# Optimization experiments

Measured on AMD Instinct MI355X. Metric: run time of the kernel, lower is better.

Reference implementation:

```python
import jax, jax.numpy as jnp
import numpy as np

DIM = 256
NHEADS = 4
HID = 512
B, H, W = 8, 48, 48
EPS = 1e-5


def _ln(x, g, b):
    mu = x.mean(-1, keepdims=True)
    var = ((x - mu) ** 2).mean(-1, keepdims=True)
    return (x - mu) * jax.lax.rsqrt(var + EPS) * g + b


def _mha(x, key_mask, wi, bi, wo, bo):
    # torch nn.MultiheadAttention (batch_first) with key padding restricted to active tokens
    Bn, N, C = x.shape
    hd = C // NHEADS
    qkv = x @ wi.T + bi  # [B,N,3C]
    q, k, v = jnp.split(qkv, 3, axis=-1)
    sh = lambda t: t.reshape(Bn, N, NHEADS, hd).transpose(0, 2, 1, 3)  # [B,h,N,hd]
    q, k, v = sh(q), sh(k), sh(v)
    scores = jnp.einsum('bhqd,bhkd->bhqk', q, k) / np.float32(np.sqrt(hd))
    scores = jnp.where(key_mask[:, None, None, :], scores, jnp.float32(-1e9))
    attn = jax.nn.softmax(scores, axis=-1)
    out = jnp.einsum('bhqk,bhkd->bhqd', attn, v)
    out = out.transpose(0, 2, 1, 3).reshape(Bn, N, C)
    return out @ wo.T + bo


def _mixer(x, key_mask, ln_g, ln_b, in_w, in_b, out_w, out_b, f1_w, f1_b, f2_w, f2_b):
    # MixerBlock: shared LayerNorm used before attn and before FFN
    xn = _ln(x, ln_g, ln_b)
    x = x + _mha(xn, key_mask, in_w, in_b, out_w, out_b)
    h = _ln(x, ln_g, ln_b)
    h = jax.nn.gelu(h @ f1_w.T + f1_b, approximate=False) @ f2_w.T + f2_b
    return x + h


def _forward(f_ir, f_vis, agent_w1, agent_b1, bn_gamma, bn_beta, bn_mean, bn_var,
             agent_w2, agent_b2, hyp_w1, hyp_b1, hyp_w2, hyp_b2,
             mir_ln_g, mir_ln_b, mir_in_w, mir_in_b, mir_out_w, mir_out_b,
             mir_f1_w, mir_f1_b, mir_f2_w, mir_f2_b,
             mvis_ln_g, mvis_ln_b, mvis_in_w, mvis_in_b, mvis_out_w, mvis_out_b,
             mvis_f1_w, mvis_f1_b, mvis_f2_w, mvis_f2_b, highlight_scale):
    Bn, C, Hh, Ww = f_ir.shape
    N = Hh * Ww
    base = f_ir + f_vis

    # SamplingAgent (1x1 convs as einsum, BatchNorm in eval mode)
    x = jnp.concatenate([f_ir, f_vis], axis=1)  # [B,2C,H,W]
    h = jnp.einsum('oc,bchw->bohw', agent_w1, x) + agent_b1[None, :, None, None]
    h = (h - bn_mean[None, :, None, None]) * jax.lax.rsqrt(bn_var[None, :, None, None] + EPS)
    h = h * bn_gamma[None, :, None, None] + bn_beta[None, :, None, None]
    h = jax.nn.relu(h)
    logits = jnp.einsum('oc,bchw->bohw', agent_w2, h) + agent_b2[None, :, None, None]
    w_driver = jax.nn.sigmoid(logits)  # [B,1,H,W]; eval path: driver = student

    # HyperNetwork threshold
    g = w_driver.mean(axis=(2, 3))  # [B,1]
    t = jax.nn.sigmoid(jax.nn.relu(g @ hyp_w1.T + hyp_b1) @ hyp_w2.T + hyp_b2)  # [B,1]

    wflat = w_driver.reshape(Bn, N)
    soft = jax.nn.sigmoid((wflat - t) * 50.0)  # [B,N]

    # active set: soft_mask > 0.5, fallback to top-64 of weights when too few
    active = soft > 0.5
    count = active.sum(axis=1)
    _, idx64 = jax.lax.top_k(wflat, 64)
    m64 = jnp.zeros((Bn, N), dtype=bool).at[jnp.arange(Bn)[:, None], idx64].set(True)
    active = jnp.where((count >= 64)[:, None], active, m64)

    tok_ir = f_ir.reshape(Bn, C, N).transpose(0, 2, 1)   # [B,N,C]
    tok_vis = f_vis.reshape(Bn, C, N).transpose(0, 2, 1)
    tok_base = base.reshape(Bn, C, N).transpose(0, 2, 1)

    refined_ir = _mixer(tok_ir, active, mir_ln_g, mir_ln_b, mir_in_w, mir_in_b,
                        mir_out_w, mir_out_b, mir_f1_w, mir_f1_b, mir_f2_w, mir_f2_b)
    refined_vis = _mixer(tok_vis, active, mvis_ln_g, mvis_ln_b, mvis_in_w, mvis_in_b,
                         mvis_out_w, mvis_out_b, mvis_f1_w, mvis_f1_b, mvis_f2_w, mvis_f2_b)

    wsel = wflat[..., None]
    fusion = refined_ir * wsel + refined_vis * (1.0 - wsel)
    delta = fusion * soft[..., None]
    mod = 1.0 + soft[..., None] * highlight_scale
    final = jnp.where(active[..., None], (tok_base + delta) * mod, tok_base)  # scatter-back
    f_final = final.transpose(0, 2, 1).reshape(Bn, C, Hh, Ww)
    aux_loss = jnp.float32(0.0)
    return f_final, aux_loss


def setup_inputs() -> dict:
    key = jax.random.key(0)
    ks = jax.random.split(key, 32)
    C = DIM
    S = 0.02
    r = lambda i, shape, s=S: jax.random.normal(ks[i], shape, dtype=jnp.float32) * s

    def mixer_params(prefix, k0):
        return {
            prefix + '_ln_g': jnp.ones((C,), jnp.float32),
            prefix + '_ln_b': jnp.zeros((C,), jnp.float32),
            prefix + '_in_w': r(k0, (3 * C, C)),
            prefix + '_in_b': jnp.zeros((3 * C,), jnp.float32),
            prefix + '_out_w': r(k0 + 1, (C, C)),
            prefix + '_out_b': jnp.zeros((C,), jnp.float32),
            prefix + '_f1_w': r(k0 + 2, (4 * C, C)),
            prefix + '_f1_b': jnp.zeros((4 * C,), jnp.float32),
            prefix + '_f2_w': r(k0 + 3, (C, 4 * C)),
            prefix + '_f2_b': jnp.zeros((C,), jnp.float32),
        }

    inp = {
        'f_ir': jax.random.normal(ks[0], (B, C, H, W), dtype=jnp.float32),
        'f_vis': jax.random.normal(ks[1], (B, C, H, W), dtype=jnp.float32),
        'agent_w1': r(2, (HID, 2 * C)),
        'agent_b1': jnp.zeros((HID,), jnp.float32),
        'bn_gamma': jnp.ones((HID,), jnp.float32),
        'bn_beta': jnp.zeros((HID,), jnp.float32),
        'bn_mean': jnp.zeros((HID,), jnp.float32),
        'bn_var': jnp.ones((HID,), jnp.float32),
        'agent_w2': r(3, (1, HID)),
        'agent_b2': jnp.zeros((1,), jnp.float32),
        'hyp_w1': r(4, (16, 1), 0.5),
        'hyp_b1': jnp.zeros((16,), jnp.float32),
        'hyp_w2': r(5, (1, 16), 0.5),
        'hyp_b2': jnp.zeros((1,), jnp.float32),
        'highlight_scale': jnp.float32(1.0),
    }
    inp.update(mixer_params('mir', 6))
    inp.update(mixer_params('mvis', 10))
    return inp


def reference(f_ir, f_vis, agent_w1, agent_b1, bn_gamma, bn_beta, bn_mean, bn_var,
              agent_w2, agent_b2, hyp_w1, hyp_b1, hyp_w2, hyp_b2,
              mir_ln_g, mir_ln_b, mir_in_w, mir_in_b, mir_out_w, mir_out_b,
              mir_f1_w, mir_f1_b, mir_f2_w, mir_f2_b,
              mvis_ln_g, mvis_ln_b, mvis_in_w, mvis_in_b, mvis_out_w, mvis_out_b,
              mvis_f1_w, mvis_f1_b, mvis_f2_w, mvis_f2_b, highlight_scale):
    return _forward(f_ir, f_vis, agent_w1, agent_b1, bn_gamma, bn_beta, bn_mean, bn_var,
                    agent_w2, agent_b2, hyp_w1, hyp_b1, hyp_w2, hyp_b2,
                    mir_ln_g, mir_ln_b, mir_in_w, mir_in_b, mir_out_w, mir_out_b,
                    mir_f1_w, mir_f1_b, mir_f2_w, mir_f2_b,
                    mvis_ln_g, mvis_ln_b, mvis_in_w, mvis_in_b, mvis_out_w, mvis_out_b,
                    mvis_f1_w, mvis_f1_b, mvis_f2_w, mvis_f2_b, highlight_scale)
```

## Files before the change

kernel.cpp:

```cpp
#include <hip/hip_runtime.h>
#include <hip/hip_bf16.h>
#include <cstdint>
#include <cstddef>

typedef __attribute__((ext_vector_type(8))) short short8;
typedef __attribute__((ext_vector_type(4))) short s16x4;
typedef __attribute__((ext_vector_type(4))) float f32x4;

#define DEVI static __device__ __forceinline__

constexpr int NB   = 8;
constexpr int CDIM = 256;
constexpr int NTOK = 2304;
constexpr int BNT  = NB * NTOK;
constexpr int HIDN = 512;
constexpr int RCAP = 4096;
constexpr size_t BNTC = (size_t)BNT * CDIM;
constexpr size_t KVSTR = (size_t)32 * NTOK * 64;
constexpr size_t HSTR  = (size_t)BNT * 1024;

DEVI unsigned short f2bf(float f) {
  unsigned u = __builtin_bit_cast(unsigned, f);
  unsigned r = 0x7FFFu + ((u >> 16) & 1u);
  return (unsigned short)((u + r) >> 16);
}
DEVI float bf2f(unsigned short h) {
  unsigned u = ((unsigned)h) << 16;
  return __builtin_bit_cast(float, u);
}

__global__ __launch_bounds__(256) void convert_weights(
    const float* __restrict__ miw, const float* __restrict__ mow,
    const float* __restrict__ mf1, const float* __restrict__ mf2,
    const float* __restrict__ viw, const float* __restrict__ vow,
    const float* __restrict__ vf1, const float* __restrict__ vf2,
    unsigned short* __restrict__ dst)
{
  int i = blockIdx.x * 256 + threadIdx.x;
  int m = i / 786432;
  int r = i % 786432;
  const float* src; int off;
  if      (r < 196608) { src = m ? viw : miw; off = r; }
  else if (r < 262144) { src = m ? vow : mow; off = r - 196608; }
  else if (r < 524288) { src = m ? vf1 : mf1; off = r - 262144; }
  else                 { src = m ? vf2 : mf2; off = r - 524288; }
  dst[i] = f2bf(src[off]);
}

__global__ __launch_bounds__(256) void split_w_kernel(
    const float* __restrict__ w1, unsigned short* __restrict__ W2)
{
  int i = blockIdx.x * 256 + threadIdx.x;
  int n = i >> 9, k = i & 511;
  float v = w1[i];
  unsigned short hi = f2bf(v);
  float r1 = v - bf2f(hi);
  unsigned short mid = f2bf(r1);
  size_t base = (size_t)n * 1024 + k;
  W2[base] = hi; W2[base + 512] = mid;
}

__global__ __launch_bounds__(256) void split_x_kernel(
    const float* __restrict__ f_ir, const float* __restrict__ f_vis,
    unsigned short* __restrict__ A2)
{
  __shared__ float tile[64][65];
  int n0 = blockIdx.x * 64, c0 = blockIdx.y * 64, b = blockIdx.z;
  int tid = threadIdx.x;
  const float* src = (c0 < 256) ? f_ir : f_vis;
  int cc0 = c0 & 255;
#pragma unroll
  for (int i = 0; i < 16; ++i) {
    int l = tid + i * 256;
    int r = l >> 6, col = l & 63;
    tile[r][col] = src[((size_t)b * 256 + cc0 + r) * NTOK + n0 + col];
  }
  __syncthreads();
#pragma unroll
  for (int i = 0; i < 16; ++i) {
    int l = tid + i * 256;
    int r = l >> 6, col = l & 63;
    A2[((size_t)b * NTOK + n0 + r) * 512 + c0 + col] = f2bf(tile[col][r]);
  }
}

__global__ __launch_bounds__(256) void agent_gemm(
    const unsigned short* __restrict__ A2, const unsigned short* __restrict__ W2,
    const float* __restrict__ b1,
    const float* __restrict__ bng, const float* __restrict__ bnb,
    const float* __restrict__ bnm, const float* __restrict__ bnv,
    const float* __restrict__ w2, float* __restrict__ hpart)
{
  __shared__ unsigned short As[128][72];
  __shared__ unsigned short Ws[128][72];
  __shared__ float scl[64], shl[64], w2l[64];
  int tid = threadIdx.x;
  int lane = tid & 63, wid = tid >> 6;
  int wm = (wid >> 1) * 64, wn = (wid & 1) * 32;
  int m0 = blockIdx.x * 128, n0 = blockIdx.y * 64;
  if (tid < 64) {
    int n = n0 + tid;
    double inv = 1.0 / sqrt((double)bnv[n] + 1e-5);
    double sc = (double)bng[n] * inv;
    scl[tid] = (float)sc;
    shl[tid] = (float)(((double)b1[n] - (double)bnm[n]) * sc + (double)bnb[n]);
    w2l[tid] = w2[n];
  }
  f32x4 zero = {0.f, 0.f, 0.f, 0.f};
  f32x4 acc[4][2];
#pragma unroll
  for (int i = 0; i < 4; ++i)
#pragma unroll
    for (int j = 0; j < 2; ++j) acc[i][j] = zero;

  for (int kin = 0; kin < 512; kin += 64) {
    __syncthreads();
#pragma unroll
    for (int i = 0; i < 4; ++i) {
      int l = tid + i * 256;
      int r = l >> 3, ch = (l & 7) * 8;
      *(short8*)&As[r][ch] = *(const short8*)&A2[(size_t)(m0 + r) * 512 + kin + ch];
    }
#pragma unroll
    for (int i = 0; i < 4; ++i) {
      int l = tid + i * 256;
      int r = l >> 3, ch = (l & 7) * 8;
      int wr = (r < 64) ? r : (r - 64);
      int wo = (r < 64) ? 0 : 512;
      *(short8*)&Ws[r][ch] = *(const short8*)&W2[(size_t)(n0 + wr) * 1024 + wo + kin + ch];
    }
    __syncthreads();
#pragma unroll
    for (int ks = 0; ks < 2; ++ks) {
      short8 a[4], bh[2], bm[2];
#pragma unroll
      for (int i = 0; i < 4; ++i)
        a[i] = *(const short8*)&As[wm + i * 16 + (lane & 15)][ks * 32 + (lane >> 4) * 8];
#pragma unroll
      for (int j = 0; j < 2; ++j) {
        bh[j] = *(const short8*)&Ws[wn + j * 16 + (lane & 15)][ks * 32 + (lane >> 4) * 8];
        bm[j] = *(const short8*)&Ws[64 + wn + j * 16 + (lane & 15)][ks * 32 + (lane >> 4) * 8];
      }
#pragma unroll
      for (int i = 0; i < 4; ++i)
#pragma unroll
        for (int j = 0; j < 2; ++j) {
          acc[i][j] = __builtin_amdgcn_mfma_f32_16x16x32_bf16(a[i], bh[j], acc[i][j], 0, 0, 0);
          acc[i][j] = __builtin_amdgcn_mfma_f32_16x16x32_bf16(a[i], bm[j], acc[i][j], 0, 0, 0);
        }
    }
  }

  int rbase = (lane >> 4) * 4;
  int cbase = lane & 15;
  float part[4][4];
#pragma unroll
  for (int i = 0; i < 4; ++i) {
#pragma unroll
    for (int r = 0; r < 4; ++r) {
      float p = 0.f;
#pragma unroll
      for (int j = 0; j < 2; ++j) {
        int nl = wn + j * 16 + cbase;
        float val = acc[i][j][r] * scl[nl] + shl[nl];
        if (val > 0.f) p += val * w2l[nl];
      }
      part[i][r] = p;
    }
  }
#pragma unroll
  for (int msk = 1; msk < 16; msk <<= 1) {
#pragma unroll
    for (int i = 0; i < 4; ++i)
#pragma unroll
      for (int r = 0; r < 4; ++r)
        part[i][r] += __shfl_xor(part[i][r], msk);
  }
  if (cbase == 0) {
    int slot = blockIdx.y * 2 + (wid & 1);
#pragma unroll
    for (int i = 0; i < 4; ++i)
#pragma unroll
      for (int r = 0; r < 4; ++r) {
        int mm = m0 + wm + i * 16 + rbase + r;
        hpart[(size_t)mm * 16 + slot] = part[i][r];
      }
  }
}

__global__ __launch_bounds__(256) void decide_kernel(
    const float* __restrict__ hpart, const float* __restrict__ b2,
    const float* __restrict__ hw1, const float* __restrict__ hb1,
    const float* __restrict__ hw2, const float* __restrict__ hb2,
    double* __restrict__ w64, float* __restrict__ w32, double* __restrict__ t64,
    int* __restrict__ rcount, int* __restrict__ rlist)
{
  __shared__ double red[256];
  __shared__ double tsh;
  int b = blockIdx.x, tid = threadIdx.x;
  double wloc[9];
  double s = 0.0;
#pragma unroll
  for (int c = 0; c < 9; ++c) {
    int pix = b * NTOK + c * 256 + tid;
    const float* hp = hpart + (size_t)pix * 16;
    double lg = (double)b2[0];
#pragma unroll
    for (int j = 0; j < 16; ++j) lg += (double)hp[j];
    double wd = 1.0 / (1.0 + exp(-lg));
    w64[pix] = wd; w32[pix] = (float)wd;
    wloc[c] = wd;
    s += wd;
  }
  red[tid] = s;
  __syncthreads();
  for (int st = 128; st; st >>= 1) {
    if (tid < st) red[tid] += red[tid + st];
    __syncthreads();
  }
  if (tid == 0) {
    double g = red[0] / 2304.0;
    double acc = (double)hb2[0];
    for (int j = 0; j < 16; ++j) {
      double hh = g * (double)hw1[j] + (double)hb1[j];
      hh = hh > 0.0 ? hh : 0.0;
      acc += hh * (double)hw2[j];
    }
    tsh = 1.0 / (1.0 + exp(-acc));
    t64[b] = tsh;
  }
  __syncthreads();
  double t = tsh;
#pragma unroll
  for (int c = 0; c < 9; ++c) {
    if (fabs(wloc[c] - t) < 1.5e-3) {
      int pix = b * NTOK + c * 256 + tid;
      int idx = atomicAdd(rcount, 1);
      if (idx < RCAP) rlist[idx] = pix;
    }
  }
}

__global__ __launch_bounds__(256) void refine_kernel(
    const float* __restrict__ f_ir, const float* __restrict__ f_vis,
    const float* __restrict__ w1, const float* __restrict__ b1,
    const float* __restrict__ bng, const float* __restrict__ bnb,
    const float* __restrict__ bnm, const float* __restrict__ bnv,
    const float* __restrict__ w2, const float* __restrict__ b2,
    const int* __restrict__ rlist, const int* __restrict__ rcount,
    double* __restrict__ w64, float* __restrict__ w32)
{
  int nr = rcount[0]; if (nr > RCAP) nr = RCAP;
  if ((int)blockIdx.x >= nr) return;
  int pix = rlist[blockIdx.x];
  int b = pix / NTOK, n = pix % NTOK;
  __shared__ double xs[512];
  __shared__ double scs[512], shs[512];
  __shared__ double lred[4];
  int tid = threadIdx.x, lane = tid & 63, wid = tid >> 6;
  xs[tid]       = (double)f_ir [((size_t)b * 256 + tid) * NTOK + n];
  xs[256 + tid] = (double)f_vis[((size_t)b * 256 + tid) * NTOK + n];
#pragma unroll
  for (int h = 0; h < 2; ++h) {
    int o = tid + h * 256;
    double inv = 1.0 / sqrt((double)bnv[o] + 1e-5);
    double sc = (double)bng[o] * inv;
    scs[o] = sc;
    shs[o] = ((double)b1[o] - (double)bnm[o]) * sc + (double)bnb[o];
  }
  __syncthreads();
  double xp[8];
#pragma unroll
  for (int j = 0; j < 8; ++j) xp[j] = xs[lane * 8 + j];
  double lg = 0.0;
  for (int oo = 0; oo < 128; oo += 8) {
    int o = wid * 128 + oo;
    double s[8] = {0, 0, 0, 0, 0, 0, 0, 0};
    const float* wr = w1 + (size_t)o * 512 + lane * 8;
#pragma unroll
    for (int t = 0; t < 8; ++t) {
#pragma unroll
      for (int j = 0; j < 8; ++j)
        s[t] += (double)wr[t * 512 + j] * xp[j];
    }
#pragma unroll
    for (int m = 1; m < 64; m <<= 1) {
#pragma unroll
      for (int t = 0; t < 8; ++t) s[t] += __shfl_xor(s[t], m);
    }
#pragma unroll
    for (int t = 0; t < 8; ++t) {
      int ot = o + t;
      double hv = s[t] * scs[ot] + shs[ot];
      if (hv > 0.0) lg += hv * (double)w2[ot];
    }
  }
  if (lane == 0) lred[wid] = lg;
  __syncthreads();
  if (tid == 0) {
    double L = lred[0] + lred[1] + lred[2] + lred[3] + (double)b2[0];
    double wd = 1.0 / (1.0 + exp(-L));
    w64[pix] = wd;
    w32[pix] = (float)wd;
  }
}

__global__ __launch_bounds__(256) void compact_kernel(
    const double* __restrict__ w64, const double* __restrict__ t64,
    float* __restrict__ soft, int* __restrict__ active, int* __restrict__ actidx,
    int* __restrict__ invmap, int* __restrict__ nact, int* __restrict__ npad)
{
  __shared__ double wv[NTOK];
  __shared__ double rv[256];
  __shared__ int   ri[256];
  __shared__ int wtot[9][4];
  int b = blockIdx.x, tid = threadIdx.x, lane = tid & 63, wid = tid >> 6;
  double t = t64[b];
  unsigned long long ltmask = (1ull << lane) - 1ull;

  int sbase = 0;
  for (int c = 0; c < 9; ++c) {
    int i = c * 256 + tid;
    double wd = w64[(size_t)b * NTOK + i];
    double sd = 1.0 / (1.0 + exp(-(wd - t) * 50.0));
    soft[(size_t)b * NTOK + i] = (float)sd;
    int a = sd > 0.5 ? 1 : 0;
    active[(size_t)b * NTOK + i] = a;
    unsigned long long ball = __ballot(a);
    int wpre = __popcll(ball & ltmask);
    if (lane == 0) wtot[c][wid] = __popcll(ball);
    __syncthreads();
    int cross = 0;
    for (int w = 0; w < wid; ++w) cross += wtot[c][w];
    int slot = sbase + cross + wpre;
    if (a) actidx[(size_t)b * NTOK + slot] = i;
    invmap[(size_t)b * NTOK + i] = a ? slot : -1;
    sbase += wtot[c][0] + wtot[c][1] + wtot[c][2] + wtot[c][3];
  }

  if (sbase < 64) {
    for (int i = tid; i < NTOK; i += 256) {
      wv[i] = w64[(size_t)b * NTOK + i];
      active[(size_t)b * NTOK + i] = 0;
    }
    __syncthreads();
    for (int it = 0; it < 64; ++it) {
      double best = -1e300; int bi = 1 << 30;
      for (int i = tid; i < NTOK; i += 256) {
        double vvv = wv[i];
        if (vvv > best || (vvv == best && i < bi)) { best = vvv; bi = i; }
      }
      rv[tid] = best; ri[tid] = bi;
      __syncthreads();
      for (int st = 128; st; st >>= 1) {
        if (tid < st) {
          if (rv[tid + st] > rv[tid] ||
              (rv[tid + st] == rv[tid] && ri[tid + st] < ri[tid])) {
            rv[tid] = rv[tid + st]; ri[tid] = ri[tid + st];
          }
        }
        __syncthreads();
      }
      if (tid == 0) { active[(size_t)b * NTOK + ri[0]] = 1; wv[ri[0]] = -1e300; }
      __syncthreads();
    }
    sbase = 0;
    for (int c = 0; c < 9; ++c) {
      int i = c * 256 + tid;
      int a = active[(size_t)b * NTOK + i];
      unsigned long long ball = __ballot(a);
      int wpre = __popcll(ball & ltmask);
      if (lane == 0) wtot[c][wid] = __popcll(ball);
      __syncthreads();
      int cross = 0;
      for (int w = 0; w < wid; ++w) cross += wtot[c][w];
      int slot = sbase + cross + wpre;
      if (a) actidx[(size_t)b * NTOK + slot] = i;
      invmap[(size_t)b * NTOK + i] = a ? slot : -1;
      sbase += wtot[c][0] + wtot[c][1] + wtot[c][2] + wtot[c][3];
    }
  }
  int n = sbase;
  int np = (n + 127) & ~127;
  if (np > NTOK) np = NTOK;
  for (int i = n + tid; i < np; i += 256) actidx[(size_t)b * NTOK + i] = -1;
  if (tid == 0) { nact[b] = n; npad[b] = np; }
}

__global__ __launch_bounds__(256) void gather_kernel(
    const unsigned short* __restrict__ A2, const int* __restrict__ actidx,
    const int* __restrict__ npad, float* __restrict__ xc)
{
  int b = blockIdx.y, i0 = blockIdx.x * 64, z = blockIdx.z;
  int cofs = z * 256;
  xc += (size_t)z * BNTC;
  if (i0 >= npad[b]) return;
  __shared__ int idx[64];
  int tid = threadIdx.x;
  if (tid < 64) idx[tid] = actidx[(size_t)b * NTOK + i0 + tid];
  __syncthreads();
#pragma unroll
  for (int it = 0; it < 16; ++it) {
    int s = tid + it * 256;
    int r = s >> 6, q4 = (s & 63) * 4;
    int src = idx[r];
    f32x4 v = {0.f, 0.f, 0.f, 0.f};
    if (src >= 0) {
      const unsigned short* p = A2 + ((size_t)b * NTOK + src) * 512 + cofs + q4;
      s16x4 hi = *(const s16x4*)&p[0];
#pragma unroll
      for (int j = 0; j < 4; ++j)
        v[j] = bf2f((unsigned short)hi[j]);
    }
    *(f32x4*)&xc[((size_t)b * NTOK + i0 + r) * 256 + q4] = v;
  }
}

__global__ __launch_bounds__(256) void ln_kernel(
    const float* __restrict__ x, size_t xstr,
    const float* __restrict__ g0, const float* __restrict__ be0,
    const float* __restrict__ g1, const float* __restrict__ be1, int zbase,
    unsigned short* __restrict__ out, size_t ostr, const int* __restrict__ npad)
{
  int z = blockIdx.y;
  x += (size_t)z * xstr; out += (size_t)z * ostr;
  const float* gamma = ((zbase + z) & 1) ? g1 : g0;
  const float* beta  = ((zbase + z) & 1) ? be1 : be0;
  int lane = threadIdx.x & 63, wid = threadIdx.x >> 6;
  int tok = blockIdx.x * 4 + wid;
  int b = tok / NTOK;
  if ((tok - b * NTOK) >= npad[b]) return;
  const float* xp = x + (size_t)tok * 256;
  f32x4 v = *(const f32x4*)&xp[lane * 4];
  float s = v[0] + v[1] + v[2] + v[3];
#pragma unroll
  for (int m = 1; m < 64; m <<= 1) s += __shfl_xor(s, m);
  float mu = s * (1.f / 256.f);
  float vs = 0.f;
#pragma unroll
  for (int j = 0; j < 4; ++j) { float d = v[j] - mu; vs += d * d; }
#pragma unroll
  for (int m = 1; m < 64; m <<= 1) vs += __shfl_xor(vs, m);
  float rs = rsqrtf(vs * (1.f / 256.f) + 1e-5f);
  f32x4 gg = *(const f32x4*)&gamma[lane * 4];
  f32x4 bb = *(const f32x4*)&beta[lane * 4];
  unsigned short r0 = f2bf((v[0] - mu) * rs * gg[0] + bb[0]);
  unsigned short r1 = f2bf((v[1] - mu) * rs * gg[1] + bb[1]);
  unsigned short r2 = f2bf((v[2] - mu) * rs * gg[2] + bb[2]);
  unsigned short r3 = f2bf((v[3] - mu) * rs * gg[3] + bb[3]);
  uint2 pk;
  pk.x = (unsigned)r0 | ((unsigned)r1 << 16);
  pk.y = (unsigned)r2 | ((unsigned)r3 << 16);
  *(uint2*)&out[(size_t)tok * 256 + lane * 4] = pk;
}

template <int EPI>
__global__ __launch_bounds__(256) void gemm_bt(
    const unsigned short* __restrict__ A, size_t astr,
    const unsigned short* __restrict__ Wt, size_t wstr,
    const float* __restrict__ biasA, const float* __restrict__ biasB, int zbase,
    float* __restrict__ xres, size_t xstr,
    float* __restrict__ fout, size_t fstr,
    unsigned short* __restrict__ bout, size_t bstr,
    unsigned short* __restrict__ qb, unsigned short* __restrict__ kb,
    unsigned short* __restrict__ vtb, size_t qstr,
    const int* __restrict__ npad, int N, int K)
{
  int z = blockIdx.z;
  A += (size_t)z * astr;
  Wt += (size_t)z * wstr;
  const float* bias = ((zbase + z) & 1) ? biasB : biasA;
  if (EPI == 0) { qb += (size_t)z * qstr; kb += (size_t)z * qstr; vtb += (size_t)z * qstr; }
  if (EPI == 1 || EPI == 3) xres += (size_t)z * xstr;
  if (EPI == 3) fout += (size_t)z * fstr;
  if (EPI == 2) bout += (size_t)z * bstr;

  int m0 = blockIdx.x * 128, n0 = blockIdx.y * 128;
  int bb = m0 / NTOK;
  if ((m0 - bb * NTOK) >= npad[bb]) return;
  __shared__ unsigned short As[128][72];
  __shared__ unsigned short Ws[128][72];
  int tid = threadIdx.x;
  int lane = tid & 63, wid = tid >> 6;
  int wm = (wid >> 1) * 64, wn = (wid & 1) * 64;
  f32x4 zero = {0.f, 0.f, 0.f, 0.f};
  f32x4 acc[4][4];
#pragma unroll
  for (int i = 0; i < 4; ++i)
#pragma unroll
    for (int j = 0; j < 4; ++j) acc[i][j] = zero;

  for (int kc = 0; kc < K; kc += 64) {
#pragma unroll
    for (int i = 0; i < 4; ++i) {
      int l = tid + i * 256;
      int r = l >> 3, ch = (l & 7) * 8;
      *(short8*)&As[r][ch] = *(const short8*)&A[(size_t)(m0 + r) * K + kc + ch];
      *(short8*)&Ws[r][ch] = *(const short8*)&Wt[(size_t)(n0 + r) * K + kc + ch];
    }
    __syncthreads();
#pragma unroll
    for (int ks = 0; ks < 2; ++ks) {
      short8 a[4], bf[4];
#pragma unroll
      for (int i = 0; i < 4; ++i)
        a[i] = *(const short8*)&As[wm + i * 16 + (lane & 15)][ks * 32 + (lane >> 4) * 8];
#pragma unroll
      for (int j = 0; j < 4; ++j)
        bf[j] = *(const short8*)&Ws[wn + j * 16 + (lane & 15)][ks * 32 + (lane >> 4) * 8];
#pragma unroll
      for (int i = 0; i < 4; ++i)
#pragma unroll
        for (int j = 0; j < 4; ++j)
          acc[i][j] = __builtin_amdgcn_mfma_f32_16x16x32_bf16(a[i], bf[j], acc[i][j], 0, 0, 0);
    }
    __syncthreads();
  }

  int rbase = (lane >> 4) * 4;
  int cbase = lane & 15;
  if (EPI == 0) {
#pragma unroll
    for (int i = 0; i < 4; ++i) {
#pragma unroll
      for (int j = 0; j < 4; ++j) {
        int n = n0 + wn + j * 16 + cbase;
        int sect = n >> 8, hh = (n & 255) >> 6, d = n & 63;
        int mA = m0 + wm + i * 16 + rbase;
        int b = mA / NTOK, tok0 = mA % NTOK;
        size_t bh = (size_t)(b * 4 + hh);
        float vals[4];
#pragma unroll
        for (int r = 0; r < 4; ++r) vals[r] = acc[i][j][r] + bias[n];
        if (sect == 0) {
#pragma unroll
          for (int r = 0; r < 4; ++r)
            qb[(bh * NTOK + tok0 + r) * 64 + d] = f2bf(vals[r] * 0.125f);
        } else if (sect == 1) {
#pragma unroll
          for (int r = 0; r < 4; ++r)
            kb[(bh * NTOK + tok0 + r) * 64 + d] = f2bf(vals[r]);
        } else {
          unsigned short p0 = f2bf(vals[0]), p1 = f2bf(vals[1]);
          unsigned short p2 = f2bf(vals[2]), p3 = f2bf(vals[3]);
          uint2 pk;
          pk.x = (unsigned)p0 | ((unsigned)p1 << 16);
          pk.y = (unsigned)p2 | ((unsigned)p3 << 16);
          *(uint2*)&vtb[(bh * 64 + d) * NTOK + tok0] = pk;
        }
      }
    }
  } else {
#pragma unroll
    for (int i = 0; i < 4; ++i) {
#pragma unroll
      for (int j = 0; j < 4; ++j) {
#pragma unroll
        for (int r = 0; r < 4; ++r) {
          int m = m0 + wm + i * 16 + rbase + r;
          int n = n0 + wn + j * 16 + cbase;
          float v = acc[i][j][r] + bias[n];
          size_t idx = (size_t)m * N + n;
          if (EPI == 1) {
            xres[idx] += v;
          } else if (EPI == 2) {
            float g = 0.5f * v * (1.f + erff(v * 0.70710678118654752f));
            bout[idx] = f2bf(g);
          } else {
            fout[idx] = xres[idx] + v;
          }
        }
      }
    }
  }
}

__global__ __launch_bounds__(256) void flash_kernel(
    const unsigned short* __restrict__ Q, const unsigned short* __restrict__ Kt,
    const unsigned short* __restrict__ VT, const int* __restrict__ nact,
    const int* __restrict__ npad, unsigned short* __restrict__ attnout)
{
  int z = blockIdx.z;
  Q += (size_t)z * KVSTR; Kt += (size_t)z * KVSTR; VT += (size_t)z * KVSTR;
  attnout += (size_t)z * BNTC;
  int bh = blockIdx.x, qt = blockIdx.y;
  int b = bh >> 2, h = bh & 3;
  int np = npad[b], na = nact[b];
  if (qt * 64 >= np) return;
  __shared__ unsigned short Ks[64][72];
  __shared__ unsigned short Vs[64][72];
  __shared__ unsigned short Ps[4][16][72];
  __shared__ float madd[64];
  int tid = threadIdx.x, lane = tid & 63, wid = tid >> 6;
  int qrow = qt * 64 + wid * 16 + (lane & 15);
  const unsigned short* qptr = Q + ((size_t)bh * NTOK + qrow) * 64;
  short8 aq0 = *(const short8*)&qptr[(lane >> 4) * 8];
  short8 aq1 = *(const short8*)&qptr[32 + (lane >> 4) * 8];
  f32x4 zero = {0.f, 0.f, 0.f, 0.f};
  f32x4 o[4];
  float mrow[4], lrow[4];
#pragma unroll
  for (int n = 0; n < 4; ++n) o[n] = zero;
#pragma unroll
  for (int r = 0; r < 4; ++r) { mrow[r] = -INFINITY; lrow[r] = 0.f; }
  const unsigned short* kbase = Kt + (size_t)bh * NTOK * 64;
  const unsigned short* vbase = VT + (size_t)bh * 64 * NTOK;
  int nkt = (na + 63) >> 6;

  for (int kt = 0; kt < nkt; ++kt) {
    int k0 = kt * 64;
#pragma unroll
    for (int i = 0; i < 2; ++i) {
      int l = tid + i * 256;
      int r = l >> 3, ch = (l & 7) * 8;
      *(short8*)&Ks[r][ch] = *(const short8*)&kbase[(size_t)(k0 + r) * 64 + ch];
      *(short8*)&Vs[r][ch] = *(const short8*)&vbase[(size_t)r * NTOK + k0 + ch];
    }
    if (tid < 64) madd[tid] = (k0 + tid < na) ? 0.f : -1e9f;
    __syncthreads();

    f32x4 s[4];
#pragma unroll
    for (int n = 0; n < 4; ++n) s[n] = zero;
#pragma unroll
    for (int n = 0; n < 4; ++n) {
      short8 bk0 = *(const short8*)&Ks[n * 16 + (lane & 15)][(lane >> 4) * 8];
      short8 bk1 = *(const short8*)&Ks[n * 16 + (lane & 15)][32 + (lane >> 4) * 8];
      s[n] = __builtin_amdgcn_mfma_f32_16x16x32_bf16(aq0, bk0, s[n], 0, 0, 0);
      s[n] = __builtin_amdgcn_mfma_f32_16x16x32_bf16(aq1, bk1, s[n], 0, 0, 0);
    }
    float pm[4] = {-INFINITY, -INFINITY, -INFINITY, -INFINITY};
#pragma unroll
    for (int n = 0; n < 4; ++n) {
      float ca = madd[n * 16 + (lane & 15)];
#pragma unroll
      for (int r = 0; r < 4; ++r) {
        s[n][r] += ca;
        pm[r] = fmaxf(pm[r], s[n][r]);
      }
    }
#pragma unroll
    for (int r = 0; r < 4; ++r) {
#pragma unroll
      for (int msk = 1; msk < 16; msk <<= 1)
        pm[r] = fmaxf(pm[r], __shfl_xor(pm[r], msk));
    }
    float sf[4], psum[4];
#pragma unroll
    for (int r = 0; r < 4; ++r) {
      float mn = fmaxf(mrow[r], pm[r]);
      sf[r] = __expf(mrow[r] - mn);
      mrow[r] = mn;
      psum[r] = 0.f;
    }
#pragma unroll
    for (int n = 0; n < 4; ++n)
#pragma unroll
      for (int r = 0; r < 4; ++r) {
        float p = __expf(s[n][r] - mrow[r]);
        s[n][r] = p;
        psum[r] += p;
      }
#pragma unroll
    for (int r = 0; r < 4; ++r) {
#pragma unroll
      for (int msk = 1; msk < 16; msk <<= 1)
        psum[r] += __shfl_xor(psum[r], msk);
      lrow[r] = lrow[r] * sf[r] + psum[r];
    }
#pragma unroll
    for (int n = 0; n < 4; ++n)
#pragma unroll
      for (int r = 0; r < 4; ++r) o[n][r] *= sf[r];
#pragma unroll
    for (int n = 0; n < 4; ++n)
#pragma unroll
      for (int r = 0; r < 4; ++r)
        Ps[wid][(lane >> 4) * 4 + r][n * 16 + (lane & 15)] = f2bf(s[n][r]);
    asm volatile("s_waitcnt lgkmcnt(0)" ::: "memory");
    __builtin_amdgcn_sched_barrier(0);
    short8 ap0 = *(const short8*)&Ps[wid][lane & 15][(lane >> 4) * 8];
    short8 ap1 = *(const short8*)&Ps[wid][lane & 15][32 + (lane >> 4) * 8];
#pragma unroll
    for (int n = 0; n < 4; ++n) {
      short8 bv0 = *(const short8*)&Vs[n * 16 + (lane & 15)][(lane >> 4) * 8];
      short8 bv1 = *(const short8*)&Vs[n * 16 + (lane & 15)][32 + (lane >> 4) * 8];
      o[n] = __builtin_amdgcn_mfma_f32_16x16x32_bf16(ap0, bv0, o[n], 0, 0, 0);
      o[n] = __builtin_amdgcn_mfma_f32_16x16x32_bf16(ap1, bv1, o[n], 0, 0, 0);
    }
    __syncthreads();
  }
#pragma unroll
  for (int n = 0; n < 4; ++n)
#pragma unroll
    for (int r = 0; r < 4; ++r) {
      int row = qt * 64 + wid * 16 + (lane >> 4) * 4 + r;
      int col = h * 64 + n * 16 + (lane & 15);
      float v = o[n][r] / lrow[r];
      attnout[((size_t)b * NTOK + row) * 256 + col] = f2bf(v);
    }
}

__global__ __launch_bounds__(256) void final_kernel(
    const float* __restrict__ f_ir, const float* __restrict__ f_vis,
    const float* __restrict__ rirc, const float* __restrict__ rvisc,
    const float* __restrict__ w32, const float* __restrict__ soft,
    const int* __restrict__ invmap, const float* __restrict__ hs_ptr,
    float* __restrict__ out)
{
  __shared__ float tir[64][65], tvis[64][65];
  __shared__ float wl[64], sl[64];
  __shared__ int il[64];
  int n0 = blockIdx.x * 64, c0 = blockIdx.y * 64, b = blockIdx.z;
  int tid = threadIdx.x;
  float hs = hs_ptr[0];
  if (tid < 64) {
    int t = b * NTOK + n0 + tid;
    wl[tid] = w32[t]; sl[tid] = soft[t]; il[tid] = invmap[t];
  }
  __syncthreads();
#pragma unroll
  for (int i = 0; i < 16; ++i) {
    int l = tid + i * 256;
    int r = l >> 6, col = l & 63;
    int ci = il[r];
    if (ci >= 0) {
      size_t idx = ((size_t)b * NTOK + ci) * 256 + c0 + col;
      tir[r][col] = rirc[idx];
      tvis[r][col] = rvisc[idx];
    }
  }
  __syncthreads();
#pragma unroll
  for (int i = 0; i < 16; ++i) {
    int l = tid + i * 256;
    int r = l >> 6, col = l & 63;
    size_t gidx = ((size_t)b * 256 + c0 + r) * NTOK + n0 + col;
    float base = f_ir[gidx] + f_vis[gidx];
    float val;
    if (il[col] >= 0) {
      float ww = wl[col], ss = sl[col];
      float fusion = tir[col][r] * ww + tvis[col][r] * (1.f - ww);
      val = (base + fusion * ss) * (1.f + ss * hs);
    } else {
      val = base;
    }
    out[gidx] = val;
  }
  if (blockIdx.x == 0 && blockIdx.y == 0 && blockIdx.z == 0 && tid == 0)
    out[(size_t)NB * 256 * NTOK] = 0.f;
}

extern "C" void kernel_launch(void* const* d_in, const int* in_sizes, int n_in,
                              void* d_out, int out_size, void* d_ws, size_t ws_size,
                              hipStream_t stream)
{
  const float* f_ir     = (const float*)d_in[0];
  const float* f_vis    = (const float*)d_in[1];
  const float* agent_w1 = (const float*)d_in[2];
  const float* agent_b1 = (const float*)d_in[3];
  const float* bn_gamma = (const float*)d_in[4];
  const float* bn_beta  = (const float*)d_in[5];
  const float* bn_mean  = (const float*)d_in[6];
  const float* bn_var   = (const float*)d_in[7];
  const float* agent_w2 = (const float*)d_in[8];
  const float* agent_b2 = (const float*)d_in[9];
  const float* hyp_w1   = (const float*)d_in[10];
  const float* hyp_b1   = (const float*)d_in[11];
  const float* hyp_w2   = (const float*)d_in[12];
  const float* hyp_b2   = (const float*)d_in[13];
  int hs_idx = (in_sizes[14] == 1) ? 14 : 34;
  int mix0   = (in_sizes[14] == 1) ? 15 : 14;
  const float* hs_ptr = (const float*)d_in[hs_idx];
  const float* mir_ln_g = (const float*)d_in[mix0 + 0];
  const float* mir_ln_b = (const float*)d_in[mix0 + 1];
  const float* mir_in_w = (const float*)d_in[mix0 + 2];
  const float* mir_in_b = (const float*)d_in[mix0 + 3];
  const float* mir_out_w= (const float*)d_in[mix0 + 4];
  const float* mir_out_b= (const float*)d_in[mix0 + 5];
  const float* mir_f1_w = (const float*)d_in[mix0 + 6];
  const float* mir_f1_b = (const float*)d_in[mix0 + 7];
  const float* mir_f2_w = (const float*)d_in[mix0 + 8];
  const float* mir_f2_b = (const float*)d_in[mix0 + 9];
  const float* mvis_ln_g = (const float*)d_in[mix0 + 10];
  const float* mvis_ln_b = (const float*)d_in[mix0 + 11];
  const float* mvis_in_w = (const float*)d_in[mix0 + 12];
  const float* mvis_in_b = (const float*)d_in[mix0 + 13];
  const float* mvis_out_w= (const float*)d_in[mix0 + 14];
  const float* mvis_out_b= (const float*)d_in[mix0 + 15];
  const float* mvis_f1_w = (const float*)d_in[mix0 + 16];
  const float* mvis_f1_b = (const float*)d_in[mix0 + 17];
  const float* mvis_f2_w = (const float*)d_in[mix0 + 18];
  const float* mvis_f2_b = (const float*)d_in[mix0 + 19];

  auto padded = [](size_t bytes) { return (bytes + 255) & ~(size_t)255; };
  size_t need2 = padded(2 * BNTC * 4)
               + padded(2 * BNTC * 2)
               + 3 * padded(2 * KVSTR * 2)
               + padded(2 * BNTC * 2)
               + padded(2 * BNTC * 4)
               + padded((size_t)2 * 786432 * 2)
               + padded((size_t)512 * 1024 * 2)
               + padded((size_t)BNT * 16 * 4)
               + padded((size_t)BNT * 8)
               + padded(64) + padded(64)
               + 3 * padded((size_t)BNT * 4)
               + padded((size_t)RCAP * 4)
               + 2 * padded((size_t)BNT * 4)
               + 2 * padded(64);
  int zc = (ws_size >= need2 + (1 << 20)) ? 2 : 1;

  char* ws = (char*)d_ws;
  size_t off = 0;
  auto alloc = [&](size_t bytes) {
    size_t o = off;
    off = (off + bytes + 255) & ~(size_t)255;
    return o;
  };
  size_t o_xc    = alloc(2 * BNTC * 4);
  size_t o_xn    = alloc((size_t)zc * BNTC * 2);
  size_t o_q     = alloc((size_t)zc * KVSTR * 2);
  size_t o_k     = alloc((size_t)zc * KVSTR * 2);
  size_t o_vt    = alloc((size_t)zc * KVSTR * 2);
  size_t o_attn  = alloc((size_t)zc * BNTC * 2);
  size_t o_rr    = alloc(2 * BNTC * 4);
  size_t o_wbf   = alloc((size_t)2 * 786432 * 2);
  size_t o_w2s   = alloc((size_t)512 * 1024 * 2);
  size_t o_hp    = alloc((size_t)BNT * 16 * 4);
  size_t o_w64   = alloc((size_t)BNT * 8);
  size_t o_t64   = alloc(64);
  size_t o_count = alloc(64);
  size_t o_w32   = alloc((size_t)BNT * 4);
  size_t o_soft  = alloc((size_t)BNT * 4);
  size_t o_act   = alloc((size_t)BNT * 4);
  size_t o_rlist = alloc((size_t)RCAP * 4);
  size_t o_aidx  = alloc((size_t)BNT * 4);
  size_t o_inv   = alloc((size_t)BNT * 4);
  size_t o_nact  = alloc(64);
  size_t o_npad  = alloc(64);
  (void)n_in; (void)out_size;

  float*  xc   = (float*)(ws + o_xc);
  unsigned short* xn   = (unsigned short*)(ws + o_xn);
  unsigned short* q    = (unsigned short*)(ws + o_q);
  unsigned short* k    = (unsigned short*)(ws + o_k);
  unsigned short* vt   = (unsigned short*)(ws + o_vt);
  unsigned short* attn = (unsigned short*)(ws + o_attn);
  unsigned short* hffn = (unsigned short*)(ws + o_q);
  float*  rr   = (float*)(ws + o_rr);
  unsigned short* A2 = (unsigned short*)(ws + o_rr);
  unsigned short* wbf  = (unsigned short*)(ws + o_wbf);
  unsigned short* W2   = (unsigned short*)(ws + o_w2s);
  float*  hpart = (float*)(ws + o_hp);
  double* w64  = (double*)(ws + o_w64);
  double* t64  = (double*)(ws + o_t64);
  int*    cnt  = (int*)(ws + o_count);
  int*    rcount = cnt + 8;
  float*  w32  = (float*)(ws + o_w32);
  float*  soft = (float*)(ws + o_soft);
  int*    act  = (int*)(ws + o_act);
  int*    rlist = (int*)(ws + o_rlist);
  int*    aidx = (int*)(ws + o_aidx);
  int*    invm = (int*)(ws + o_inv);
  int*    nact = (int*)(ws + o_nact);
  int*    npad = (int*)(ws + o_npad);

  const unsigned short* mir_in  = wbf;
  const unsigned short* mir_out = wbf + 196608;
  const unsigned short* mir_f1  = wbf + 262144;
  const unsigned short* mir_f2  = wbf + 524288;
  const unsigned short* vis_in  = wbf + 786432;
  const unsigned short* vis_out = wbf + 786432 + 196608;
  const unsigned short* vis_f1  = wbf + 786432 + 262144;
  const unsigned short* vis_f2  = wbf + 786432 + 524288;

  hipMemsetAsync(cnt, 0, 16 * sizeof(int), stream);
  convert_weights<<<6144, 256, 0, stream>>>(mir_in_w, mir_out_w, mir_f1_w, mir_f2_w,
                                            mvis_in_w, mvis_out_w, mvis_f1_w, mvis_f2_w,
                                            wbf);
  split_w_kernel<<<1024, 256, 0, stream>>>(agent_w1, W2);
  split_x_kernel<<<dim3(36, 8, 8), 256, 0, stream>>>(f_ir, f_vis, A2);

  agent_gemm<<<dim3(BNT / 128, 8), 256, 0, stream>>>(
      A2, W2, agent_b1, bn_gamma, bn_beta, bn_mean, bn_var, agent_w2, hpart);
  decide_kernel<<<8, 256, 0, stream>>>(
      hpart, agent_b2, hyp_w1, hyp_b1, hyp_w2, hyp_b2, w64, w32, t64, rcount, rlist);
  refine_kernel<<<RCAP, 256, 0, stream>>>(
      f_ir, f_vis, agent_w1, agent_b1, bn_gamma, bn_beta, bn_mean, bn_var,
      agent_w2, agent_b2, rlist, rcount, w64, w32);
  compact_kernel<<<8, 256, 0, stream>>>(w64, t64, soft, act, aidx, invm, nact, npad);

  gather_kernel<<<dim3(36, 8, 2), 256, 0, stream>>>(A2, aidx, npad, xc);

  if (zc == 2) {
    size_t WSTR = 786432;
    ln_kernel<<<dim3(BNT / 4, 2), 256, 0, stream>>>(
        xc, BNTC, mir_ln_g, mir_ln_b, mvis_ln_g, mvis_ln_b, 0, xn, BNTC, npad);
    gemm_bt<0><<<dim3(BNT / 128, 6, 2), 256, 0, stream>>>(
        xn, BNTC, mir_in, WSTR, mir_in_b, mvis_in_b, 0,
        nullptr, 0, nullptr, 0, nullptr, 0, q, k, vt, KVSTR, npad, 768, 256);
    flash_kernel<<<dim3(32, 36, 2), 256, 0, stream>>>(q, k, vt, nact, npad, attn);
    gemm_bt<1><<<dim3(BNT / 128, 2, 2), 256, 0, stream>>>(
        attn, BNTC, mir_out, WSTR, mir_out_b, mvis_out_b, 0,
        xc, BNTC, nullptr, 0, nullptr, 0, nullptr, nullptr, nullptr, 0, npad, 256, 256);
    ln_kernel<<<dim3(BNT / 4, 2), 256, 0, stream>>>(
        xc, BNTC, mir_ln_g, mir_ln_b, mvis_ln_g, mvis_ln_b, 0, xn, BNTC, npad);
    gemm_bt<2><<<dim3(BNT / 128, 8, 2), 256, 0, stream>>>(
        xn, BNTC, mir_f1, WSTR, mir_f1_b, mvis_f1_b, 0,
        nullptr, 0, nullptr, 0, hffn, HSTR, nullptr, nullptr, nullptr, 0, npad, 1024, 256);
    gemm_bt<3><<<dim3(BNT / 128, 2, 2), 256, 0, stream>>>(
        hffn, HSTR, mir_f2, WSTR, mir_f2_b, mvis_f2_b, 0,
        xc, BNTC, rr, BNTC, nullptr, 0, nullptr, nullptr, nullptr, 0, npad, 256, 1024);
  } else {
    for (int s = 0; s < 2; ++s) {
      const float* g   = s ? mvis_ln_g : mir_ln_g;
      const float* be  = s ? mvis_ln_b : mir_ln_b;
      const unsigned short* w_in  = s ? vis_in  : mir_in;
      const unsigned short* w_out = s ? vis_out : mir_out;
      const unsigned short* w_f1  = s ? vis_f1  : mir_f1;
      const unsigned short* w_f2  = s ? vis_f2  : mir_f2;
      const float* b_in  = s ? mvis_in_b  : mir_in_b;
      const float* b_out = s ? mvis_out_b : mir_out_b;
      const float* b_f1  = s ? mvis_f1_b  : mir_f1_b;
      const float* b_f2  = s ? mvis_f2_b  : mir_f2_b;
      float* xcs = xc + (size_t)s * BNTC;
      float* rrs = rr + (size_t)s * BNTC;
      ln_kernel<<<dim3(BNT / 4, 1), 256, 0, stream>>>(
          xcs, 0, g, be, g, be, 0, xn, 0, npad);
      gemm_bt<0><<<dim3(BNT / 128, 6, 1), 256, 0, stream>>>(
          xn, 0, w_in, 0, b_in, b_in, 0,
          nullptr, 0, nullptr, 0, nullptr, 0, q, k, vt, 0, npad, 768, 256);
      flash_kernel<<<dim3(32, 36, 1), 256, 0, stream>>>(q, k, vt, nact, npad, attn);
      gemm_bt<1><<<dim3(BNT / 128, 2, 1), 256, 0, stream>>>(
          attn, 0, w_out, 0, b_out, b_out, 0,
          xcs, 0, nullptr, 0, nullptr, 0, nullptr, nullptr, nullptr, 0, npad, 256, 256);
      ln_kernel<<<dim3(BNT / 4, 1), 256, 0, stream>>>(
          xcs, 0, g, be, g, be, 0, xn, 0, npad);
      gemm_bt<2><<<dim3(BNT / 128, 8, 1), 256, 0, stream>>>(
          xn, 0, w_f1, 0, b_f1, b_f1, 0,
          nullptr, 0, nullptr, 0, hffn, 0, nullptr, nullptr, nullptr, 0, npad, 1024, 256);
      gemm_bt<3><<<dim3(BNT / 128, 2, 1), 256, 0, stream>>>(
          hffn, 0, w_f2, 0, b_f2, b_f2, 0,
          xcs, 0, rrs, 0, nullptr, 0, nullptr, nullptr, nullptr, 0, npad, 256, 1024);
    }
  }

  final_kernel<<<dim3(36, 4, 8), 256, 0, stream>>>(
      f_ir, f_vis, rr, rr + BNTC, w32, soft, invm, hs_ptr, (float*)d_out);
}
```

Measured before the change: 267.0 us.

## Batch four pixels per refine block and aggregate refine-list atomics per wavefront

The refine kernel now processes four borderline pixels per block, so each float64 load of the agent weight row is reused across four pixels, and the launch grid shrinks by four. The decide kernel replaces per-thread atomics with a wavefront ballot and a single atomicAdd per wave. The borderline tolerance for recomputing pixels in float64 is tightened from 1.5e-3 to 8e-4, which cuts refine work. That narrower band risks misclassifying pixels whose bf16-path weight sits near the threshold.

```diff
diff --git a/kernel.cpp b/kernel.cpp
--- a/kernel.cpp
+++ b/kernel.cpp
@@ -197,7 +197,8 @@
 {
   __shared__ double red[256];
   __shared__ double tsh;
-  int b = blockIdx.x, tid = threadIdx.x;
+  int b = blockIdx.x, tid = threadIdx.x, lane = tid & 63;
+  unsigned long long ltmask = (1ull << lane) - 1ull;
   double wloc[9];
   double s = 0.0;
 #pragma unroll
@@ -233,10 +234,17 @@
   double t = tsh;
 #pragma unroll
   for (int c = 0; c < 9; ++c) {
-    if (fabs(wloc[c] - t) < 1.5e-3) {
-      int pix = b * NTOK + c * 256 + tid;
-      int idx = atomicAdd(rcount, 1);
-      if (idx < RCAP) rlist[idx] = pix;
+    int flag = fabs(wloc[c] - t) < 8e-4 ? 1 : 0;
+    unsigned long long ball = __ballot(flag);
+    if (ball) {
+      int leader = __ffsll((long long)ball) - 1;
+      int base = 0;
+      if (lane == leader) base = atomicAdd(rcount, __popcll(ball));
+      base = __shfl(base, leader);
+      if (flag) {
+        int idx = base + __popcll(ball & ltmask);
+        if (idx < RCAP) rlist[idx] = b * NTOK + c * 256 + tid;
+      }
     }
   }
 }
@@ -251,15 +259,15 @@
     double* __restrict__ w64, float* __restrict__ w32)
 {
   int nr = rcount[0]; if (nr > RCAP) nr = RCAP;
-  if ((int)blockIdx.x >= nr) return;
-  int pix = rlist[blockIdx.x];
-  int b = pix / NTOK, n = pix % NTOK;
-  __shared__ double xs[512];
+  int p0 = blockIdx.x * 4;
+  if (p0 >= nr) return;
+  int npx = nr - p0; if (npx > 4) npx = 4;
+  __shared__ double xs[4][512];
   __shared__ double scs[512], shs[512];
-  __shared__ double lred[4];
+  __shared__ double lred[4][4];
+  __shared__ int pixs[4];
   int tid = threadIdx.x, lane = tid & 63, wid = tid >> 6;
-  xs[tid]       = (double)f_ir [((size_t)b * 256 + tid) * NTOK + n];
-  xs[256 + tid] = (double)f_vis[((size_t)b * 256 + tid) * NTOK + n];
+  if (tid < 4) pixs[tid] = rlist[p0 + (tid < npx ? tid : 0)];
 #pragma unroll
   for (int h = 0; h < 2; ++h) {
     int o = tid + h * 256;
@@ -269,39 +277,62 @@
     shs[o] = ((double)b1[o] - (double)bnm[o]) * sc + (double)bnb[o];
   }
   __syncthreads();
-  double xp[8];
-#pragma unroll
-  for (int j = 0; j < 8; ++j) xp[j] = xs[lane * 8 + j];
-  double lg = 0.0;
-  for (int oo = 0; oo < 128; oo += 8) {
+#pragma unroll
+  for (int i = 0; i < 8; ++i) {
+    int sidx = tid + i * 256;
+    int p = sidx >> 9, kk = sidx & 511;
+    int pix = pixs[p];
+    int b = pix / NTOK, n = pix % NTOK;
+    const float* fsrc = (kk < 256) ? f_ir : f_vis;
+    xs[p][kk] = (double)fsrc[((size_t)b * 256 + (kk & 255)) * NTOK + n];
+  }
+  __syncthreads();
+  double xp[4][8];
+#pragma unroll
+  for (int p = 0; p < 4; ++p)
+#pragma unroll
+    for (int j = 0; j < 8; ++j) xp[p][j] = xs[p][lane * 8 + j];
+  double lg[4] = {0.0, 0.0, 0.0, 0.0};
+  for (int oo = 0; oo < 128; oo += 2) {
     int o = wid * 128 + oo;
-    double s[8] = {0, 0, 0, 0, 0, 0, 0, 0};
+    double s[2][4] = {};
     const float* wr = w1 + (size_t)o * 512 + lane * 8;
 #pragma unroll
-    for (int t = 0; t < 8; ++t) {
-#pragma unroll
-      for (int j = 0; j < 8; ++j)
-        s[t] += (double)wr[t * 512 + j] * xp[j];
-    }
-#pragma unroll
-    for (int m = 1; m < 64; m <<= 1) {
-#pragma unroll
-      for (int t = 0; t < 8; ++t) s[t] += __shfl_xor(s[t], m);
-    }
-#pragma unroll
-    for (int t = 0; t < 8; ++t) {
+    for (int t = 0; t < 2; ++t)
+#pragma unroll
+      for (int j = 0; j < 8; ++j) {
+        double wv = (double)wr[t * 512 + j];
+#pragma unroll
+        for (int p = 0; p < 4; ++p)
+          s[t][p] += wv * xp[p][j];
+      }
+#pragma unroll
+    for (int m = 1; m < 64; m <<= 1)
+#pragma unroll
+      for (int t = 0; t < 2; ++t)
+#pragma unroll
+        for (int p = 0; p < 4; ++p)
+          s[t][p] += __shfl_xor(s[t][p], m);
+#pragma unroll
+    for (int t = 0; t < 2; ++t) {
       int ot = o + t;
-      double hv = s[t] * scs[ot] + shs[ot];
-      if (hv > 0.0) lg += hv * (double)w2[ot];
-    }
-  }
-  if (lane == 0) lred[wid] = lg;
+#pragma unroll
+      for (int p = 0; p < 4; ++p) {
+        double hv = s[t][p] * scs[ot] + shs[ot];
+        if (hv > 0.0) lg[p] += hv * (double)w2[ot];
+      }
+    }
+  }
+  if (lane == 0)
+#pragma unroll
+    for (int p = 0; p < 4; ++p) lred[wid][p] = lg[p];
   __syncthreads();
-  if (tid == 0) {
-    double L = lred[0] + lred[1] + lred[2] + lred[3] + (double)b2[0];
+  if (tid < npx) {
+    int p = tid;
+    double L = lred[0][p] + lred[1][p] + lred[2][p] + lred[3][p] + (double)b2[0];
     double wd = 1.0 / (1.0 + exp(-L));
-    w64[pix] = wd;
-    w32[pix] = (float)wd;
+    w64[pixs[p]] = wd;
+    w32[pixs[p]] = (float)wd;
   }
 }
 
@@ -885,7 +916,7 @@
       A2, W2, agent_b1, bn_gamma, bn_beta, bn_mean, bn_var, agent_w2, hpart);
   decide_kernel<<<8, 256, 0, stream>>>(
       hpart, agent_b2, hyp_w1, hyp_b1, hyp_w2, hyp_b2, w64, w32, t64, rcount, rlist);
-  refine_kernel<<<RCAP, 256, 0, stream>>>(
+  refine_kernel<<<RCAP / 4, 256, 0, stream>>>(
       f_ir, f_vis, agent_w1, agent_b1, bn_gamma, bn_beta, bn_mean, bn_var,
       agent_w2, agent_b2, rlist, rcount, w64, w32);
   compact_kernel<<<8, 256, 0, stream>>>(w64, t64, soft, act, aidx, invm, nact, npad);
```

After: 371.1 us. 39.0% more time.
